# Kernel tuning notes

Measured on AMD Instinct MI355X. Metric: run time of the kernel, lower is better.

Reference implementation:

```python
import jax, jax.numpy as jnp
import numpy as np

EMBED_DIM = 1024
NUM_HEADS = 16
HEAD_DIM = EMBED_DIM // NUM_HEADS


def setup_inputs() -> dict:
    key = jax.random.key(0)
    ks = jax.random.split(key, 9)
    B, S, D = 2, 2048, EMBED_DIM
    scale = 1.0 / np.sqrt(D)
    x = jax.random.normal(ks[0], (B, S, D), dtype=jnp.float32)
    # Linear params (torch nn.Linear: y = x @ W.T + b); store W as [out, in]
    Wq = jax.random.normal(ks[1], (D, D), dtype=jnp.float32) * scale
    bq = jnp.zeros((D,), dtype=jnp.float32)
    Wk = jax.random.normal(ks[2], (D, D), dtype=jnp.float32) * scale
    bk = jnp.zeros((D,), dtype=jnp.float32)
    Wv = jax.random.normal(ks[3], (D, D), dtype=jnp.float32) * scale
    bv = jnp.zeros((D,), dtype=jnp.float32)
    Wo = jax.random.normal(ks[4], (D, D), dtype=jnp.float32) * scale
    bo = jnp.zeros((D,), dtype=jnp.float32)
    return {"x": x, "Wq": Wq, "bq": bq, "Wk": Wk, "bk": bk,
            "Wv": Wv, "bv": bv, "Wo": Wo, "bo": bo}


def reference(x, Wq, bq, Wk, bk, Wv, bv, Wo, bo):
    B, S, D = x.shape
    H, Hd = NUM_HEADS, HEAD_DIM
    scaling = Hd ** -0.5
    # projections (torch Linear: x @ W.T + b)
    q = (x @ Wq.T + bq).reshape(B, S, H, Hd).transpose(0, 2, 1, 3)  # [B,H,S,Hd]
    k = (x @ Wk.T + bk).reshape(B, S, H, Hd).transpose(0, 2, 1, 3)
    v = (x @ Wv.T + bv).reshape(B, S, H, Hd).transpose(0, 2, 1, 3)
    # full score matrix, as in the original (no flash tiling)
    scores = jnp.einsum('bhqd,bhkd->bhqk', q, k) * scaling  # [B,H,S,S]
    attn = jax.nn.softmax(scores, axis=-1)
    # dropout is identity in eval mode
    out = jnp.einsum('bhqk,bhkd->bhqd', attn, v)  # [B,H,S,Hd]
    out = out.transpose(0, 2, 1, 3).reshape(B, S, D)
    return out @ Wo.T + bo
```

## Files before the change

kernel.cpp:

```cpp
#include <hip/hip_runtime.h>
#include <stdint.h>

typedef unsigned short u16;
typedef short short8 __attribute__((ext_vector_type(8)));
typedef float f32x4 __attribute__((ext_vector_type(4)));
typedef float f32x16 __attribute__((ext_vector_type(16)));
typedef float f32x2 __attribute__((ext_vector_type(2)));

__device__ __forceinline__ u16 f2bf_fast(float f) {
  union { float f; uint32_t u; } x;
  x.f = f;
  return (u16)((x.u + 0x8000u) >> 16);
}

__device__ __forceinline__ uint32_t pack2bf(float lo, float hi) {
  union { float f; uint32_t u; } a, b;
  a.f = lo; b.f = hi;
  return __builtin_amdgcn_perm(b.u + 0x8000u, a.u + 0x8000u, 0x07060302u);
}

__device__ __forceinline__ float bf2f(uint32_t u) {
  union { uint32_t u; float f; } x;
  x.u = u << 16;
  return x.f;
}

__device__ __forceinline__ uint32_t cvtpk(float lo, float hi) {
  uint32_t r;
  asm("v_cvt_pk_bf16_f32 %0, %1, %2" : "=v"(r) : "v"(lo), "v"(hi));
  return r;
}

__device__ __forceinline__ void permswap(uint32_t& a, uint32_t& b) {
  asm("v_permlane32_swap_b32 %0, %1" : "+v"(a), "+v"(b));
}

__device__ __forceinline__ void gload_lds16(const void* g, void* l) {
  __builtin_amdgcn_global_load_lds(
      (const __attribute__((address_space(1))) void*)g,
      (__attribute__((address_space(3))) void*)l, 16, 0, 0);
}

__device__ __forceinline__ f32x4 mfma16(short8 a, short8 b, f32x4 c) {
  return __builtin_amdgcn_mfma_f32_16x16x32_bf16(a, b, c, 0, 0, 0);
}

__device__ __forceinline__ f32x16 mfma32(short8 a, short8 b, f32x16 c) {
  return __builtin_amdgcn_mfma_f32_32x32x16_bf16(a, b, c, 0, 0, 0);
}

#define QSCALE 0.18033688011112042f

__global__ void pack_all(const float* __restrict__ x, const float* __restrict__ wq,
                         const float* __restrict__ wk, const float* __restrict__ wv,
                         const float* __restrict__ wo, u16* __restrict__ xp,
                         u16* __restrict__ wp) {
  const int gi = blockIdx.x * 256 + threadIdx.x;
  const int lane = gi & 63;
  const int kc = (gi >> 6) & 31;
  const int rt = gi >> 11;
  const int col = kc * 32 + (lane >> 4) * 8;
  const float* src;
  int row;
  if (rt < 256) {
    src = x;
    row = rt * 16 + (lane & 15);
  } else {
    const int wti = rt - 256;
    const int widx = wti >> 6;
    src = (widx == 0) ? wq : (widx == 1) ? wk : (widx == 2) ? wv : wo;
    row = (wti & 63) * 16 + (lane & 15);
  }
  const float4* p = (const float4*)(src + (size_t)row * 1024 + col);
  const float4 v0 = p[0], v1 = p[1];
  uint4 o;
  o.x = pack2bf(v0.x, v0.y);
  o.y = pack2bf(v0.z, v0.w);
  o.z = pack2bf(v1.x, v1.y);
  o.w = pack2bf(v1.z, v1.w);
  u16* dst = (rt < 256) ? xp : wp;
  const int og = (rt < 256) ? gi : gi - 524288;
  ((uint4*)dst)[og] = o;
}

__global__ __launch_bounds__(256, 3) void proj_qkv(
    const u16* __restrict__ xp, const u16* __restrict__ wp,
    const float* __restrict__ bq, const float* __restrict__ bk,
    const float* __restrict__ bv, u16* __restrict__ qw, u16* __restrict__ kw,
    u16* __restrict__ vw) {
  __shared__ __align__(16) u16 As[8192];
  __shared__ __align__(16) u16 Bs[8192];
  const int tid = threadIdx.x, lane = tid & 63, w = tid >> 6;
  const int quad = lane >> 4, l15 = lane & 15;

  const int bid = blockIdx.x;
  const int work = (bid & 7) * 96 + (bid >> 3);
  const bool isQK = work < 512;
  int at0, bt0, bm2, bn2;
  const u16 *Ap, *Bp;
  if (isQK) {
    bm2 = work >> 4; bn2 = work & 15;
    Ap = xp; at0 = bm2 * 8;
    Bp = wp; bt0 = bn2 * 8;
  } else {
    const int h = work - 512;
    bm2 = h >> 5; bn2 = h & 31;
    Ap = wp; at0 = 128 + bm2 * 8;
    Bp = xp; bt0 = bn2 * 8;
  }
  const int wr = w >> 1, wc = w & 1;
  const int bm = bm2 * 2 + wr, bn = bn2 * 2 + wc;

  auto stage = [&](int kc, int buf) {
#pragma unroll
    for (int i = 0; i < 4; ++i) {
      const int g = w * 4 + i;
      const int t = g & 7;
      const u16* src = (g < 8)
          ? (Ap + (((at0 + t) << 5) + kc) * 512 + lane * 8)
          : (Bp + (((bt0 + t) << 5) + kc) * 512 + lane * 8);
      u16* dst = ((g < 8) ? As : Bs) + (buf * 8 + t) * 512 + lane * 8;
      gload_lds16(src, dst);
    }
  };

  f32x4 acc[4][4] = {};

  stage(0, 0);
  __syncthreads();

  for (int kc = 0; kc < 32; ++kc) {
    const int cur = kc & 1;
    if (kc < 31) stage(kc + 1, cur ^ 1);

    const u16* Ab = As + cur * 4096;
    const u16* Bb = Bs + cur * 4096;
    short8 af[4], bf[4];
#pragma unroll
    for (int mt = 0; mt < 4; ++mt)
      af[mt] = *(const short8*)&Ab[((wr * 4 + mt) * 64 + lane) * 8];
#pragma unroll
    for (int nt = 0; nt < 4; ++nt)
      bf[nt] = *(const short8*)&Bb[((wc * 4 + nt) * 64 + lane) * 8];

#pragma unroll
    for (int mt = 0; mt < 4; ++mt)
#pragma unroll
      for (int nt = 0; nt < 4; ++nt)
        acc[mt][nt] = mfma16(af[mt], bf[nt], acc[mt][nt]);
    __syncthreads();
  }

  u16* tw = ((w < 2) ? As : Bs) + (w & 1) * 4096;
#pragma unroll
  for (int nt = 0; nt < 4; ++nt) {
    const int n = bn * 64 + nt * 16 + l15;
    float ba = 0.f, sc = 1.f;
    if (isQK) {
      if (bn < 16) { ba = bq[n] * QSCALE; sc = QSCALE; }
      else          ba = bk[n - 1024];
    }
#pragma unroll
    for (int mt = 0; mt < 4; ++mt)
#pragma unroll
      for (int r = 0; r < 4; ++r) {
        const int m = bm * 64 + mt * 16 + quad * 4 + r;
        const float v = isQK ? (acc[mt][nt][r] * sc + ba)
                             : (acc[mt][nt][r] + bv[m]);
        tw[(mt * 16 + quad * 4 + r) * 64 + nt * 16 + l15] = f2bf_fast(v);
      }
  }
  const int rr = lane >> 3, ch = lane & 7;
  if (isQK) {
    const bool isQ = (bn < 16);
    u16* op = isQ ? qw : kw;
    const int hh = isQ ? bn : bn - 16;
#pragma unroll
    for (int p = 0; p < 8; ++p) {
      const int row = p * 8 + rr;
      const int m = bm * 64 + row;
      const int b = m >> 11, s = m & 2047;
      const uint4 val = *(const uint4*)&tw[row * 64 + ch * 8];
      *(uint4*)(op + ((size_t)((b * 16 + hh) * 2048 + s)) * 64 + ch * 8) = val;
    }
  } else {
    const int nb = bn * 64;
    const int b = nb >> 11, s = nb & 2047;
#pragma unroll
    for (int p = 0; p < 8; ++p) {
      const int row = p * 8 + rr;
      const int m = bm * 64 + row;
      const uint4 val = *(const uint4*)&tw[row * 64 + ch * 8];
      *(uint4*)(vw + ((size_t)(b * 1024 + m)) * 2048 + s + ch * 8) = val;
    }
  }
}

__global__ __launch_bounds__(512, 4) void attn_kernel(
    const u16* __restrict__ Q, const u16* __restrict__ Kt,
    const u16* __restrict__ Vt, u16* __restrict__ awp) {
  __shared__ __align__(16) u16 Sm[40960];
  const int tid = threadIdx.x, lane = tid & 63, w = tid >> 6;
  const int l31 = lane & 31, hi = lane >> 5, l7 = lane & 7;
  const int kh = w >> 2, qg = w & 3;

  const int bid = blockIdx.y * 16 + blockIdx.x;
  const int work = (bid & 7) * 64 + (bid >> 3);
  const int qt = work & 15;
  const int bh = work >> 4;

  const char* Qb = (const char*)(Q + ((size_t)bh * 2048 + qt * 128) * 64);
  const char* Kb = (const char*)(Kt + (size_t)bh * 2048 * 64);
  const char* Vb = (const char*)(Vt + (size_t)bh * 64 * 2048);

  auto stageKV = [&](int j, int buf) {
#pragma unroll
    for (int h = 0; h < 2; ++h) {
      const int kt = h * 16 + j;
      u16* Kl = Sm + (buf * 2 + h) * 8192;
      u16* Vl = Kl + 4096;
      const int G = w * 64 + lane;
      const int r = G >> 3, sl = G & 7;
      gload_lds16(Kb + (size_t)(kt * 64 + r) * 128 + ((sl ^ (r & 7)) * 16),
                  &Kl[G * 8]);
      gload_lds16(Vb + (size_t)r * 4096 + kt * 128 + ((sl ^ (r & 7)) * 16),
                  &Vl[G * 8]);
    }
  };

  u16* Qs = Sm + 32768;
#pragma unroll
  for (int i = 0; i < 2; ++i) {
    const int G = (w * 2 + i) * 64 + lane;
    const int row = G >> 3, sl = G & 7;
    gload_lds16(Qb + (size_t)row * 128 + ((sl ^ (row & 7)) * 16), &Qs[G * 8]);
  }
  stageKV(0, 0);
  __syncthreads();

  short8 aq[4];
#pragma unroll
  for (int ds = 0; ds < 4; ++ds)
    aq[ds] = *(const short8*)&Qs[(qg * 32 + l31) * 64 + (((ds << 1) + hi) ^ l7) * 8];

  f32x16 ot[2] = {};
  f32x2 l2 = {0.f, 0.f};

  for (int j = 0; j < 16; ++j) {
    const int buf = j & 1;
    if (j < 15) stageKV(j + 1, buf ^ 1);
    const u16* Kl = Sm + (buf * 2 + kh) * 8192;
    const u16* Vl = Kl + 4096;

#pragma unroll
    for (int t = 0; t < 2; ++t) {
      f32x16 st = {};
      __builtin_amdgcn_s_setprio(1);
#pragma unroll
      for (int ds = 0; ds < 4; ++ds) {
        short8 kf = *(const short8*)&Kl[(t * 32 + l31) * 64 +
                                        (((ds << 1) + hi) ^ l7) * 8];
        st = mfma32(kf, aq[ds], st);
      }
      __builtin_amdgcn_s_setprio(0);
      float e[16];
#pragma unroll
      for (int i = 0; i < 16; ++i) e[i] = __builtin_amdgcn_exp2f(st[i]);
#pragma unroll
      for (int i = 0; i < 8; ++i) l2 += (f32x2){e[2 * i], e[2 * i + 1]};

      uint32_t p01 = cvtpk(e[0], e[1]),   p23 = cvtpk(e[2], e[3]);
      uint32_t p45 = cvtpk(e[4], e[5]),   p67 = cvtpk(e[6], e[7]);
      uint32_t p89 = cvtpk(e[8], e[9]),   pAB = cvtpk(e[10], e[11]);
      uint32_t pCD = cvtpk(e[12], e[13]), pEF = cvtpk(e[14], e[15]);
      permswap(p01, p45);
      permswap(p23, p67);
      permswap(p89, pCD);
      permswap(pAB, pEF);
      union { uint32_t u[4]; short8 s; } b0, b1;
      b0.u[0] = p01; b0.u[1] = p23; b0.u[2] = p45; b0.u[3] = p67;
      b1.u[0] = p89; b1.u[1] = pAB; b1.u[2] = pCD; b1.u[3] = pEF;

      __builtin_amdgcn_s_setprio(1);
#pragma unroll
      for (int dt = 0; dt < 2; ++dt) {
#pragma unroll
        for (int s2 = 0; s2 < 2; ++s2) {
          short8 vf = *(const short8*)&Vl[(dt * 32 + l31) * 64 +
                                          ((((t * 2 + s2) << 1) + hi) ^ l7) * 8];
          ot[dt] = mfma32(vf, s2 ? b1.s : b0.s, ot[dt]);
        }
      }
      __builtin_amdgcn_s_setprio(0);
    }
    if (j < 15) __syncthreads();
  }

  float l = l2.x + l2.y;
  l += __shfl_xor(l, 32);

  __syncthreads();
  float* fb = (float*)Sm;
  if (kh == 1) {
    float* p = fb + (qg * 64 + lane) * 34;
#pragma unroll
    for (int i = 0; i < 8; ++i) {
      *(f32x2*)(p + 2 * i)      = (f32x2){ot[0][2 * i], ot[0][2 * i + 1]};
      *(f32x2*)(p + 16 + 2 * i) = (f32x2){ot[1][2 * i], ot[1][2 * i + 1]};
    }
    p[32] = l;
  }
  __syncthreads();
  if (kh == 0) {
    const float* p = fb + (qg * 64 + lane) * 34;
#pragma unroll
    for (int i = 0; i < 16; ++i) ot[0][i] += p[i];
#pragma unroll
    for (int i = 0; i < 16; ++i) ot[1][i] += p[16 + i];
    l += p[32];
    const float inv = __builtin_amdgcn_rcpf(l);

    const int b = bh >> 4, h = bh & 15;
    const int rt = b * 128 + qt * 8 + qg * 2 + (l31 >> 4);
#pragma unroll
    for (int dt = 0; dt < 2; ++dt) {
      const int kc = h * 2 + dt;
#pragma unroll
      for (int g = 0; g < 4; ++g) {
        const int ln = (lane & 15) + 16 * g;
        uint2 ov;
        ov.x = cvtpk(ot[dt][4 * g + 0] * inv, ot[dt][4 * g + 1] * inv);
        ov.y = cvtpk(ot[dt][4 * g + 2] * inv, ot[dt][4 * g + 3] * inv);
        *(uint2*)(awp + ((size_t)((rt * 32 + kc) * 64 + ln)) * 8 + hi * 4) = ov;
      }
    }
  }
}

__global__ __launch_bounds__(512) void out_proj(const u16* __restrict__ awp,
                                                const u16* __restrict__ wp,
                                                const float* __restrict__ bo,
                                                float* __restrict__ out) {
  __shared__ __align__(16) u16 As[16384];
  __shared__ __align__(16) u16 Bs[8192];
  const int tid = threadIdx.x, lane = tid & 63, w = tid >> 6;
  const int quad = lane >> 4, l15 = lane & 15;

  const int bid = blockIdx.x;
  const int work = (bid & 7) * 64 + (bid >> 3);
  const int bm2 = work >> 4, bn2 = work & 15;
  const int at0 = bm2 * 8, bt0 = 192 + bn2 * 4;
  const int wr = w >> 1, wc = w & 1;

  auto stage = [&](int ks, int buf) {
    const int kc0 = ks * 2;
#pragma unroll
    for (int i = 0; i < 2; ++i) {
      const u16* src = awp + (((at0 + w) << 5) + kc0 + i) * 512 + lane * 8;
      u16* dst = As + buf * 8192 + (i * 8 + w) * 512 + lane * 8;
      gload_lds16(src, dst);
    }
    {
      const int c = w >> 2, tg = w & 3;
      const u16* src = wp + (((bt0 + tg) << 5) + kc0 + c) * 512 + lane * 8;
      u16* dst = Bs + buf * 4096 + (c * 4 + tg) * 512 + lane * 8;
      gload_lds16(src, dst);
    }
  };

  f32x4 acc[2][2] = {};

  stage(0, 0);
  __syncthreads();

  for (int ks = 0; ks < 16; ++ks) {
    const int cur = ks & 1;
    if (ks < 15) stage(ks + 1, cur ^ 1);

    const u16* Ab = As + cur * 8192;
    const u16* Bb = Bs + cur * 4096;
#pragma unroll
    for (int c = 0; c < 2; ++c) {
      short8 af[2], bf[2];
#pragma unroll
      for (int mt = 0; mt < 2; ++mt)
        af[mt] = *(const short8*)&Ab[((c * 8 + wr * 2 + mt) * 64 + lane) * 8];
#pragma unroll
      for (int nt = 0; nt < 2; ++nt)
        bf[nt] = *(const short8*)&Bb[((c * 4 + wc * 2 + nt) * 64 + lane) * 8];
#pragma unroll
      for (int mt = 0; mt < 2; ++mt)
#pragma unroll
        for (int nt = 0; nt < 2; ++nt)
          acc[mt][nt] = mfma16(af[mt], bf[nt], acc[mt][nt]);
    }
    __syncthreads();
  }

#pragma unroll
  for (int nt = 0; nt < 2; ++nt) {
    const int n = bn2 * 64 + wc * 32 + nt * 16 + l15;
    const float bb = bo[n];
#pragma unroll
    for (int mt = 0; mt < 2; ++mt)
#pragma unroll
      for (int r = 0; r < 4; ++r) {
        const int m = bm2 * 128 + wr * 32 + mt * 16 + quad * 4 + r;
        out[(size_t)m * 1024 + n] = acc[mt][nt][r] + bb;
      }
  }
}

extern "C" void kernel_launch(void* const* d_in, const int* in_sizes, int n_in,
                              void* d_out, int out_size, void* d_ws, size_t ws_size,
                              hipStream_t stream) {
  const float* x  = (const float*)d_in[0];
  const float* Wq = (const float*)d_in[1];
  const float* bq = (const float*)d_in[2];
  const float* Wk = (const float*)d_in[3];
  const float* bk = (const float*)d_in[4];
  const float* Wv = (const float*)d_in[5];
  const float* bv = (const float*)d_in[6];
  const float* Wo = (const float*)d_in[7];
  const float* bo = (const float*)d_in[8];

  const size_t M4 = (size_t)4 * 1024 * 1024;
  u16* xp  = (u16*)d_ws;
  u16* wp  = xp + M4;
  u16* qw  = wp + M4;
  u16* kw  = qw + M4;
  u16* vw  = kw + M4;
  u16* awp = vw + M4;

  pack_all<<<4096, 256, 0, stream>>>(x, Wq, Wk, Wv, Wo, xp, wp);

  proj_qkv<<<768, 256, 0, stream>>>(xp, wp, bq, bk, bv, qw, kw, vw);

  attn_kernel<<<dim3(16, 32), 512, 0, stream>>>(qw, kw, vw, awp);

  out_proj<<<512, 512, 0, stream>>>(awp, wp, bo, (float*)d_out);
}
```

Baseline: 175.9 us.

## Halve QKV projection N-tile and compute softmax row sums with MFMA

The QKV projection tile shrinks from 128x128 to 128x64, doubling the grid to 1536 blocks and reducing shared memory and accumulator registers, with the min-blocks launch bound removed. This is meant to improve occupancy and wave balance, at the cost of less data reuse per block. In the attention kernel, the per-element VALU accumulation of exp values plus a cross-lane shuffle is replaced by an MFMA against a bf16 ones vector. That moves the row-sum work onto the matrix units and sums the bf16-rounded probabilities, which is consistent with the values used in P·V.

```diff
diff --git a/kernel.cpp b/kernel.cpp
--- a/kernel.cpp
+++ b/kernel.cpp
@@ -83,48 +83,47 @@
   ((uint4*)dst)[og] = o;
 }
 
-__global__ __launch_bounds__(256, 3) void proj_qkv(
+__global__ __launch_bounds__(256) void proj_qkv(
     const u16* __restrict__ xp, const u16* __restrict__ wp,
     const float* __restrict__ bq, const float* __restrict__ bk,
     const float* __restrict__ bv, u16* __restrict__ qw, u16* __restrict__ kw,
     u16* __restrict__ vw) {
   __shared__ __align__(16) u16 As[8192];
-  __shared__ __align__(16) u16 Bs[8192];
+  __shared__ __align__(16) u16 Bs[4096];
   const int tid = threadIdx.x, lane = tid & 63, w = tid >> 6;
   const int quad = lane >> 4, l15 = lane & 15;
 
   const int bid = blockIdx.x;
-  const int work = (bid & 7) * 96 + (bid >> 3);
-  const bool isQK = work < 512;
+  const int work = (bid & 7) * 192 + (bid >> 3);
+  const bool isQK = work < 1024;
   int at0, bt0, bm2, bn2;
   const u16 *Ap, *Bp;
   if (isQK) {
-    bm2 = work >> 4; bn2 = work & 15;
+    bm2 = work >> 5; bn2 = work & 31;
     Ap = xp; at0 = bm2 * 8;
-    Bp = wp; bt0 = bn2 * 8;
+    Bp = wp; bt0 = bn2 * 4;
   } else {
-    const int h = work - 512;
-    bm2 = h >> 5; bn2 = h & 31;
+    const int h = work - 1024;
+    bm2 = h >> 6; bn2 = h & 63;
     Ap = wp; at0 = 128 + bm2 * 8;
-    Bp = xp; bt0 = bn2 * 8;
+    Bp = xp; bt0 = bn2 * 4;
   }
   const int wr = w >> 1, wc = w & 1;
-  const int bm = bm2 * 2 + wr, bn = bn2 * 2 + wc;
 
   auto stage = [&](int kc, int buf) {
 #pragma unroll
-    for (int i = 0; i < 4; ++i) {
-      const int g = w * 4 + i;
-      const int t = g & 7;
+    for (int i = 0; i < 3; ++i) {
+      const int g = w * 3 + i;
       const u16* src = (g < 8)
-          ? (Ap + (((at0 + t) << 5) + kc) * 512 + lane * 8)
-          : (Bp + (((bt0 + t) << 5) + kc) * 512 + lane * 8);
-      u16* dst = ((g < 8) ? As : Bs) + (buf * 8 + t) * 512 + lane * 8;
+          ? (Ap + (((at0 + g) << 5) + kc) * 512 + lane * 8)
+          : (Bp + (((bt0 + (g - 8)) << 5) + kc) * 512 + lane * 8);
+      u16* dst = (g < 8) ? (As + (buf * 8 + g) * 512 + lane * 8)
+                         : (Bs + (buf * 4 + (g - 8)) * 512 + lane * 8);
       gload_lds16(src, dst);
     }
   };
 
-  f32x4 acc[4][4] = {};
+  f32x4 acc[4][2] = {};
 
   stage(0, 0);
   __syncthreads();
@@ -134,64 +133,65 @@
     if (kc < 31) stage(kc + 1, cur ^ 1);
 
     const u16* Ab = As + cur * 4096;
-    const u16* Bb = Bs + cur * 4096;
-    short8 af[4], bf[4];
+    const u16* Bb = Bs + cur * 2048;
+    short8 af[4], bf[2];
 #pragma unroll
     for (int mt = 0; mt < 4; ++mt)
       af[mt] = *(const short8*)&Ab[((wr * 4 + mt) * 64 + lane) * 8];
 #pragma unroll
-    for (int nt = 0; nt < 4; ++nt)
-      bf[nt] = *(const short8*)&Bb[((wc * 4 + nt) * 64 + lane) * 8];
+    for (int nt = 0; nt < 2; ++nt)
+      bf[nt] = *(const short8*)&Bb[((wc * 2 + nt) * 64 + lane) * 8];
 
 #pragma unroll
     for (int mt = 0; mt < 4; ++mt)
 #pragma unroll
-      for (int nt = 0; nt < 4; ++nt)
+      for (int nt = 0; nt < 2; ++nt)
         acc[mt][nt] = mfma16(af[mt], bf[nt], acc[mt][nt]);
     __syncthreads();
   }
 
-  u16* tw = ((w < 2) ? As : Bs) + (w & 1) * 4096;
-#pragma unroll
-  for (int nt = 0; nt < 4; ++nt) {
-    const int n = bn * 64 + nt * 16 + l15;
+  u16* tw = As + w * 2048;
+#pragma unroll
+  for (int nt = 0; nt < 2; ++nt) {
+    const int n = bn2 * 64 + wc * 32 + nt * 16 + l15;
     float ba = 0.f, sc = 1.f;
     if (isQK) {
-      if (bn < 16) { ba = bq[n] * QSCALE; sc = QSCALE; }
-      else          ba = bk[n - 1024];
+      if (bn2 < 16) { ba = bq[n] * QSCALE; sc = QSCALE; }
+      else           ba = bk[n - 1024];
     }
 #pragma unroll
     for (int mt = 0; mt < 4; ++mt)
 #pragma unroll
       for (int r = 0; r < 4; ++r) {
-        const int m = bm * 64 + mt * 16 + quad * 4 + r;
+        const int m = bm2 * 128 + wr * 64 + mt * 16 + quad * 4 + r;
         const float v = isQK ? (acc[mt][nt][r] * sc + ba)
                              : (acc[mt][nt][r] + bv[m]);
-        tw[(mt * 16 + quad * 4 + r) * 64 + nt * 16 + l15] = f2bf_fast(v);
+        tw[(mt * 16 + quad * 4 + r) * 32 + nt * 16 + l15] = f2bf_fast(v);
       }
   }
-  const int rr = lane >> 3, ch = lane & 7;
+  const int rr = lane >> 2, ch = lane & 3;
   if (isQK) {
-    const bool isQ = (bn < 16);
+    const bool isQ = (bn2 < 16);
     u16* op = isQ ? qw : kw;
-    const int hh = isQ ? bn : bn - 16;
-#pragma unroll
-    for (int p = 0; p < 8; ++p) {
-      const int row = p * 8 + rr;
-      const int m = bm * 64 + row;
+    const int hh = isQ ? bn2 : bn2 - 16;
+#pragma unroll
+    for (int p = 0; p < 4; ++p) {
+      const int row = p * 16 + rr;
+      const int m = bm2 * 128 + wr * 64 + row;
       const int b = m >> 11, s = m & 2047;
-      const uint4 val = *(const uint4*)&tw[row * 64 + ch * 8];
-      *(uint4*)(op + ((size_t)((b * 16 + hh) * 2048 + s)) * 64 + ch * 8) = val;
+      const uint4 val = *(const uint4*)&tw[row * 32 + ch * 8];
+      *(uint4*)(op + ((size_t)((b * 16 + hh) * 2048 + s)) * 64 + wc * 32 +
+                ch * 8) = val;
     }
   } else {
-    const int nb = bn * 64;
-    const int b = nb >> 11, s = nb & 2047;
-#pragma unroll
-    for (int p = 0; p < 8; ++p) {
-      const int row = p * 8 + rr;
-      const int m = bm * 64 + row;
-      const uint4 val = *(const uint4*)&tw[row * 64 + ch * 8];
-      *(uint4*)(vw + ((size_t)(b * 1024 + m)) * 2048 + s + ch * 8) = val;
+    const int sb = bn2 * 64;
+    const int b = sb >> 11, s0 = (sb & 2047) + wc * 32;
+#pragma unroll
+    for (int p = 0; p < 4; ++p) {
+      const int row = p * 16 + rr;
+      const int m = bm2 * 128 + wr * 64 + row;
+      const uint4 val = *(const uint4*)&tw[row * 32 + ch * 8];
+      *(uint4*)(vw + ((size_t)(b * 1024 + m)) * 2048 + s0 + ch * 8) = val;
     }
   }
 }
@@ -243,8 +243,12 @@
   for (int ds = 0; ds < 4; ++ds)
     aq[ds] = *(const short8*)&Qs[(qg * 32 + l31) * 64 + (((ds << 1) + hi) ^ l7) * 8];
 
+  union { uint32_t u[4]; short8 s; } ones;
+#pragma unroll
+  for (int i = 0; i < 4; ++i) ones.u[i] = 0x3F803F80u;
+
   f32x16 ot[2] = {};
-  f32x2 l2 = {0.f, 0.f};
+  f32x16 lacc = {};
 
   for (int j = 0; j < 16; ++j) {
     const int buf = j & 1;
@@ -266,8 +270,6 @@
       float e[16];
 #pragma unroll
       for (int i = 0; i < 16; ++i) e[i] = __builtin_amdgcn_exp2f(st[i]);
-#pragma unroll
-      for (int i = 0; i < 8; ++i) l2 += (f32x2){e[2 * i], e[2 * i + 1]};
 
       uint32_t p01 = cvtpk(e[0], e[1]),   p23 = cvtpk(e[2], e[3]);
       uint32_t p45 = cvtpk(e[4], e[5]),   p67 = cvtpk(e[6], e[7]);
@@ -282,6 +284,8 @@
       b1.u[0] = p89; b1.u[1] = pAB; b1.u[2] = pCD; b1.u[3] = pEF;
 
       __builtin_amdgcn_s_setprio(1);
+      lacc = mfma32(ones.s, b0.s, lacc);
+      lacc = mfma32(ones.s, b1.s, lacc);
 #pragma unroll
       for (int dt = 0; dt < 2; ++dt) {
 #pragma unroll
@@ -296,8 +300,7 @@
     if (j < 15) __syncthreads();
   }
 
-  float l = l2.x + l2.y;
-  l += __shfl_xor(l, 32);
+  float l = lacc[0];
 
   __syncthreads();
   float* fb = (float*)Sm;
@@ -434,7 +437,7 @@
 
   pack_all<<<4096, 256, 0, stream>>>(x, Wq, Wk, Wv, Wo, xp, wp);
 
-  proj_qkv<<<768, 256, 0, stream>>>(xp, wp, bq, bk, bv, qw, kw, vw);
+  proj_qkv<<<1536, 256, 0, stream>>>(xp, wp, bq, bk, bv, qw, kw, vw);
 
   attn_kernel<<<dim3(16, 32), 512, 0, stream>>>(qw, kw, vw, awp);
 
```

After: 194.6 us. 10.6% more time.
